# Kernel optimization log

Measured on AMD Instinct MI355X. Metric: run time of the kernel, lower is better.

## Reference

```python
import jax, jax.numpy as jnp
import numpy as np

DIM = 768
HEADS = 12
HEAD_DIM = DIM // HEADS
SCALE = HEAD_DIM ** -0.5
NEG = -65504.0


def setup_inputs() -> dict:
    key = jax.random.key(0)
    ks = jax.random.split(key, 7)
    B, N, C = 8, 1024, DIM
    x = jax.random.normal(ks[0], (B, N, C), dtype=jnp.float32)
    rel_pos_bias = jax.random.normal(ks[1], (HEADS, N, N), dtype=jnp.float32)
    attn_mask = jax.random.randint(ks[2], (B, N, N), 0, 2) == 1
    # parameters (torch nn.Linear: y = x @ W.T + b)
    W_qkv = jax.random.normal(ks[3], (3 * C, C), dtype=jnp.float32) * (C ** -0.5)
    b_qkv = jnp.zeros((3 * C,), dtype=jnp.float32)
    W_proj = jax.random.normal(ks[4], (C, C), dtype=jnp.float32) * (C ** -0.5)
    b_proj = jnp.zeros((C,), dtype=jnp.float32)
    return {"x": x, "rel_pos_bias": rel_pos_bias, "attn_mask": attn_mask,
            "W_qkv": W_qkv, "b_qkv": b_qkv, "W_proj": W_proj, "b_proj": b_proj}


def reference(x, rel_pos_bias, attn_mask, W_qkv, b_qkv, W_proj, b_proj):
    B, N, C = x.shape
    qkv = x @ W_qkv.T + b_qkv                                  # [B,N,3C]
    qkv = qkv.reshape(B, N, 3, HEADS, HEAD_DIM).transpose(2, 0, 3, 1, 4)
    q, k, v = qkv[0], qkv[1], qkv[2]                           # [B,H,N,D]
    attn = jnp.einsum('bhnd,bhmd->bhnm', q * SCALE, k)         # [B,H,N,N]
    attn = jnp.where(attn_mask[:, None, :, :], NEG, attn)
    attn = attn + rel_pos_bias[None]                           # bias broadcast over B
    attn_wo_softmax = attn
    p = jax.nn.softmax(attn, axis=-1)                          # attn_drop p=0 (eval)
    out = jnp.einsum('bhnm,bhmd->bhnd', p, v)
    out = out.transpose(0, 2, 1, 3).reshape(B, N, C)
    out = out @ W_proj.T + b_proj                              # proj_drop p=0
    return out, attn_wo_softmax
```

## Files before the change

kernel.cpp:

```cpp
#include <hip/hip_runtime.h>
#include <hip/hip_bf16.h>

typedef __attribute__((ext_vector_type(8))) short bf16x8;
typedef __attribute__((ext_vector_type(4))) short bf16x4;
typedef __attribute__((ext_vector_type(4))) float f32x4;

#define MFMA32(a,b,c) __builtin_amdgcn_mfma_f32_16x16x32_bf16(a,b,c,0,0,0)

#if __has_builtin(__builtin_amdgcn_mfma_f32_16x16x16bf16_1k)
#define MFMA16(a,b,c) __builtin_amdgcn_mfma_f32_16x16x16bf16_1k(a,b,c,0,0,0)
#else
static __device__ __forceinline__ f32x4 mfma16_asm(bf16x4 a, bf16x4 b, f32x4 c){
  asm volatile("v_mfma_f32_16x16x16_bf16 %0, %1, %2, %0" : "+v"(c) : "v"(a), "v"(b));
  return c;
}
#define MFMA16(a,b,c) mfma16_asm(a,b,c)
#endif

#define NEGV -65504.0f

__device__ __forceinline__ unsigned short f2bf(float f){
  union { float f; unsigned u; } x; x.f = f;
  unsigned r = x.u + 0x7fffu + ((x.u >> 16) & 1u);
  return (unsigned short)(r >> 16);
}

__device__ __forceinline__ unsigned cvtpk(float a, float b){
  unsigned r;
  asm volatile("v_cvt_pk_bf16_f32 %0, %1, %2" : "=v"(r) : "v"(a), "v"(b));
  return r;
}

__global__ void cvt_all(const float* __restrict__ x, const float* __restrict__ wq,
                        const float* __restrict__ wp, unsigned short* __restrict__ out){
  int i = blockIdx.x * 256 + threadIdx.x;
  const float* src; int j;
  if (i < 1572864)      { src = x;  j = i; }
  else if (i < 2015232) { src = wq; j = i - 1572864; }
  else                  { src = wp; j = i - 2015232; }
  float4 f = ((const float4*)src)[j];
  ushort4 u;
  u.x = f2bf(f.x); u.y = f2bf(f.y); u.z = f2bf(f.z); u.w = f2bf(f.w);
  ((ushort4*)out)[i] = u;
}

__global__ __launch_bounds__(256) void mask_to_bits(const int* __restrict__ m,
                                                    unsigned long long* __restrict__ out){
  int gw = (blockIdx.x * 256 + threadIdx.x) >> 6;
  int lane = threadIdx.x & 63;
#pragma unroll
  for (int stp = 0; stp < 16; ++stp) {
    size_t base = ((size_t)gw * 16 + stp) * 64;
    int v = m[base + lane];
    unsigned long long bb = __ballot(v != 0);
    if (lane == 0) out[base >> 6] = bb;
  }
}

__global__ __launch_bounds__(256) void gemm_qkv(
    const unsigned short* __restrict__ X,
    const unsigned short* __restrict__ W,
    const float* __restrict__ bias,
    unsigned short* __restrict__ Qd,
    unsigned short* __restrict__ Kd,
    unsigned short* __restrict__ Vd)
{
  __shared__ unsigned short As[128*40];
  __shared__ unsigned short Bs[128*40];
  const int K = 768;
  int tid = threadIdx.x;
  int bm = blockIdx.x & 63;
  int bn = blockIdx.x >> 6;
  int wave = tid >> 6, lane = tid & 63;
  int lo = lane & 15, g = lane >> 4;
  int wr = (wave >> 1) * 64, wc = (wave & 1) * 64;
  int row0 = bm * 128, col0 = bn * 128;

  int sr = tid >> 1;
  int sc = (tid & 1) * 16;
  const unsigned short* gA = X + (size_t)(row0 + sr) * K + sc;
  const unsigned short* gB = W + (size_t)(col0 + sr) * K + sc;
  unsigned short* sA = &As[sr * 40 + sc];
  unsigned short* sB = &Bs[sr * 40 + sc];

  f32x4 acc[4][4] = {};
  for (int k0 = 0; k0 < K; k0 += 32) {
    bf16x8 a0 = *(const bf16x8*)(gA + k0);
    bf16x8 a1 = *(const bf16x8*)(gA + k0 + 8);
    bf16x8 b0 = *(const bf16x8*)(gB + k0);
    bf16x8 b1 = *(const bf16x8*)(gB + k0 + 8);
    __syncthreads();
    *(bf16x8*)(sA)     = a0;
    *(bf16x8*)(sA + 8) = a1;
    *(bf16x8*)(sB)     = b0;
    *(bf16x8*)(sB + 8) = b1;
    __syncthreads();
    bf16x8 af[4], bf[4];
#pragma unroll
    for (int i = 0; i < 4; ++i) af[i] = *(const bf16x8*)&As[(wr + i*16 + lo)*40 + g*8];
#pragma unroll
    for (int i = 0; i < 4; ++i) bf[i] = *(const bf16x8*)&Bs[(wc + i*16 + lo)*40 + g*8];
#pragma unroll
    for (int mi = 0; mi < 4; ++mi)
#pragma unroll
      for (int ni = 0; ni < 4; ++ni)
        acc[mi][ni] = MFMA32(af[mi], bf[ni], acc[mi][ni]);
  }
  int orow0 = row0 + wr, ocol0 = col0 + wc;
#pragma unroll
  for (int ni = 0; ni < 4; ++ni) {
    int col = ocol0 + ni*16 + lo;
    float bc = bias[col];
    int which = col / 768;
    int rem = col - which * 768;
    int h = rem >> 6, d = rem & 63;
    unsigned short* dst = (which == 0) ? Qd : (which == 1) ? Kd : Vd;
    float scale = (which == 0) ? 0.125f : 1.0f;
#pragma unroll
    for (int mi = 0; mi < 4; ++mi) {
#pragma unroll
      for (int r = 0; r < 4; ++r) {
        int row = orow0 + mi*16 + g*4 + r;
        int bb = row >> 10, n = row & 1023;
        dst[(((size_t)bb*12 + h)*1024 + n)*64 + d] = f2bf((acc[mi][ni][r] + bc) * scale);
      }
    }
  }
}

__global__ __launch_bounds__(256) void vtrans(const unsigned short* __restrict__ V,
                                              unsigned short* __restrict__ Vt){
  __shared__ unsigned short t[64][72];
  int bh = blockIdx.y;
  int n0 = blockIdx.x * 64;
  int tid = threadIdx.x;
  int nl = tid >> 2;
  int dq = (tid & 3) * 16;
  const unsigned short* src = V + ((size_t)bh*1024 + n0 + nl)*64 + dq;
  bf16x8 a0 = *(const bf16x8*)(src);
  bf16x8 a1 = *(const bf16x8*)(src + 8);
  *(bf16x8*)&t[nl][dq]     = a0;
  *(bf16x8*)&t[nl][dq + 8] = a1;
  __syncthreads();
  int d  = tid >> 2;
  int nq = (tid & 3) * 16;
  union { unsigned short s[16]; bf16x8 v[2]; } pk;
#pragma unroll
  for (int j = 0; j < 16; ++j) pk.s[j] = t[nq + j][d];
  unsigned short* dst = Vt + ((size_t)bh*64 + d)*1024 + n0 + nq;
  *(bf16x8*)(dst)     = pk.v[0];
  *(bf16x8*)(dst + 8) = pk.v[1];
}

__global__ __launch_bounds__(512, 4) void attn_kernel(
    const unsigned short* __restrict__ Qd,
    const unsigned short* __restrict__ Kd,
    const unsigned short* __restrict__ Vt,
    const float* __restrict__ bias,
    const unsigned* __restrict__ maskbits,
    float* __restrict__ out1,
    unsigned short* __restrict__ ctx)
{
  __shared__ char lds[32768];
  const int N = 1024, D = 64;
  int y = blockIdx.y;
  int h = y >> 3, bb = y & 7;
  int bh = bb * 12 + h;
  int tid = threadIdx.x;
  int wave = tid >> 6, lane = tid & 63;
  int lo = lane & 15, g = lane >> 4;
  int qrow = blockIdx.x * 128 + wave * 16 + lo;

  const size_t qoff = ((size_t)bh * N + qrow) * D;
  bf16x8 qf0 = *(const bf16x8*)(Qd + qoff + g*8);
  bf16x8 qf1 = *(const bf16x8*)(Qd + qoff + 32 + g*8);

  const float* bias_row = bias + ((size_t)h * N + qrow) * N;
  const unsigned* mrow  = maskbits + ((size_t)bb * N + qrow) * 32;
  float* out_row        = out1 + ((size_t)bh * N + qrow) * N;

  int o  = tid * 16;
  int sw = o ^ (((o >> 7) & 7) << 4);
  const char* kbase = (const char*)(Kd + (size_t)bh * N * D);
  const char* vbase = (const char*)(Vt + (size_t)bh * D * N);
  const char* ksrc  = kbase + sw;
  const char* vsrc  = vbase + (o >> 7) * 2048 + (sw & 127);
  int wbase = (tid >> 6) << 10;

#define STAGE(buf, kv) do { \
    __builtin_amdgcn_global_load_lds( \
      (const __attribute__((address_space(1))) unsigned*)(ksrc + (size_t)(kv)*128), \
      (__attribute__((address_space(3))) unsigned*)(lds + (buf)*8192 + wbase), 16, 0, 0); \
    __builtin_amdgcn_global_load_lds( \
      (const __attribute__((address_space(1))) unsigned*)(vsrc + (size_t)(kv)*2), \
      (__attribute__((address_space(3))) unsigned*)(lds + 16384 + (buf)*8192 + wbase), 16, 0, 0); \
  } while (0)

#define SWZ(lb) ((lb) ^ ((((lb) >> 7) & 7) << 4))

  float m_run = -INFINITY, l_part = 0.0f;
  f32x4 oacc[4] = {};

  STAGE(0, 0);
  __syncthreads();
  int cur = 0;

  for (int it = 0; it < 16; ++it) {
    int kv = it * 64;
    if (it < 15) STAGE(cur ^ 1, kv + 64);
    __builtin_amdgcn_sched_barrier(0);

    unsigned mw0 = mrow[it*2];
    unsigned mw1 = mrow[it*2 + 1];

    f32x4 s[4];
    __builtin_amdgcn_s_setprio(1);
#pragma unroll
    for (int sub = 0; sub < 4; ++sub) {
      int lbr = (sub*16 + lo) * 128 + g*16;
      bf16x8 k0 = *(const bf16x8*)(lds + cur*8192 + SWZ(lbr));
      bf16x8 k1 = *(const bf16x8*)(lds + cur*8192 + SWZ(lbr + 64));
      f32x4 t = {};
      t = MFMA32(k0, qf0, t);
      t = MFMA32(k1, qf1, t);
      s[sub] = t;
    }
    __builtin_amdgcn_s_setprio(0);

    float sp[16];
#pragma unroll
    for (int sub = 0; sub < 4; ++sub) {
      f32x4 bi = *(const f32x4*)(bias_row + kv + sub*16 + g*4);
      unsigned mw = (sub < 2) ? mw0 : mw1;
      int sh = (sub & 1) * 16 + g * 4;
#pragma unroll
      for (int r = 0; r < 4; ++r)
        sp[sub*4+r] = (((mw >> (sh + r)) & 1u) ? NEGV : s[sub][r]) + bi[r];
      f32x4 ov;
      ov[0] = sp[sub*4]; ov[1] = sp[sub*4+1]; ov[2] = sp[sub*4+2]; ov[3] = sp[sub*4+3];
      __builtin_nontemporal_store(ov, (f32x4*)(out_row + kv + sub*16 + g*4));
    }

    float lmax = sp[0];
#pragma unroll
    for (int i = 1; i < 16; ++i) lmax = fmaxf(lmax, sp[i]);
    if (!__all(lmax <= m_run + 8.0f)) {
      float tmax = fmaxf(lmax, __shfl_xor(lmax, 16));
      tmax = fmaxf(tmax, __shfl_xor(tmax, 32));
      float mnew = fmaxf(m_run, tmax);
      float alpha = __expf(m_run - mnew);
      l_part *= alpha;
#pragma unroll
      for (int c = 0; c < 4; ++c) {
        oacc[c][0] *= alpha; oacc[c][1] *= alpha;
        oacc[c][2] *= alpha; oacc[c][3] *= alpha;
      }
      m_run = mnew;
    }
    float lsum = 0.0f;
#pragma unroll
    for (int i = 0; i < 16; ++i) { sp[i] = __expf(sp[i] - m_run); lsum += sp[i]; }
    l_part += lsum;

    union { unsigned u[2]; bf16x4 h; } pk[4];
#pragma unroll
    for (int ks = 0; ks < 4; ++ks) {
      pk[ks].u[0] = cvtpk(sp[ks*4],   sp[ks*4+1]);
      pk[ks].u[1] = cvtpk(sp[ks*4+2], sp[ks*4+3]);
    }

    __builtin_amdgcn_s_setprio(1);
#pragma unroll
    for (int ks = 0; ks < 4; ++ks)
#pragma unroll
      for (int c = 0; c < 4; ++c) {
        int lbv = (c*16 + lo) * 128 + ks*32 + g*8;
        bf16x4 vf = *(const bf16x4*)(lds + 16384 + cur*8192 + SWZ(lbv));
        oacc[c] = MFMA16(vf, pk[ks].h, oacc[c]);
      }
    __builtin_amdgcn_s_setprio(0);

    cur ^= 1;
    __builtin_amdgcn_sched_barrier(0);
    asm volatile("s_waitcnt vmcnt(4)" ::: "memory");
    __builtin_amdgcn_s_barrier();
  }

  l_part += __shfl_xor(l_part, 16);
  l_part += __shfl_xor(l_part, 32);
  float inv = 1.0f / l_part;

  size_t crow = ((size_t)bb * N + qrow) * 768 + h * 64;
#pragma unroll
  for (int c = 0; c < 4; ++c) {
    ushort4 u;
    u.x = f2bf(oacc[c][0] * inv);
    u.y = f2bf(oacc[c][1] * inv);
    u.z = f2bf(oacc[c][2] * inv);
    u.w = f2bf(oacc[c][3] * inv);
    *(ushort4*)(ctx + crow + c*16 + g*4) = u;
  }
#undef STAGE
#undef SWZ
}

__global__ __launch_bounds__(256) void gemm_proj(
    const unsigned short* __restrict__ X,
    const unsigned short* __restrict__ W,
    const float* __restrict__ bias,
    float* __restrict__ out)
{
  __shared__ unsigned short As[128*40];
  __shared__ unsigned short Bs[128*40];
  const int K = 768;
  int tid = threadIdx.x;
  int bm = blockIdx.x & 63;
  int bn = blockIdx.x >> 6;
  int wave = tid >> 6, lane = tid & 63;
  int lo = lane & 15, g = lane >> 4;
  int wr = (wave >> 1) * 64, wc = (wave & 1) * 64;
  int row0 = bm * 128, col0 = bn * 128;

  int sr = tid >> 1;
  int sc = (tid & 1) * 16;
  const unsigned short* gA = X + (size_t)(row0 + sr) * K + sc;
  const unsigned short* gB = W + (size_t)(col0 + sr) * K + sc;
  unsigned short* sA = &As[sr * 40 + sc];
  unsigned short* sB = &Bs[sr * 40 + sc];

  f32x4 acc[4][4] = {};
  for (int k0 = 0; k0 < K; k0 += 32) {
    bf16x8 a0 = *(const bf16x8*)(gA + k0);
    bf16x8 a1 = *(const bf16x8*)(gA + k0 + 8);
    bf16x8 b0 = *(const bf16x8*)(gB + k0);
    bf16x8 b1 = *(const bf16x8*)(gB + k0 + 8);
    __syncthreads();
    *(bf16x8*)(sA)     = a0;
    *(bf16x8*)(sA + 8) = a1;
    *(bf16x8*)(sB)     = b0;
    *(bf16x8*)(sB + 8) = b1;
    __syncthreads();
    bf16x8 af[4], bf[4];
#pragma unroll
    for (int i = 0; i < 4; ++i) af[i] = *(const bf16x8*)&As[(wr + i*16 + lo)*40 + g*8];
#pragma unroll
    for (int i = 0; i < 4; ++i) bf[i] = *(const bf16x8*)&Bs[(wc + i*16 + lo)*40 + g*8];
#pragma unroll
    for (int mi = 0; mi < 4; ++mi)
#pragma unroll
      for (int ni = 0; ni < 4; ++ni)
        acc[mi][ni] = MFMA32(af[mi], bf[ni], acc[mi][ni]);
  }
  int orow0 = row0 + wr, ocol0 = col0 + wc;
#pragma unroll
  for (int ni = 0; ni < 4; ++ni) {
    int col = ocol0 + ni*16 + lo;
    float bc = bias[col];
#pragma unroll
    for (int mi = 0; mi < 4; ++mi) {
#pragma unroll
      for (int r = 0; r < 4; ++r) {
        int row = orow0 + mi*16 + g*4 + r;
        out[(size_t)row * 768 + col] = acc[mi][ni][r] + bc;
      }
    }
  }
}

extern "C" void kernel_launch(void* const* d_in, const int* in_sizes, int n_in,
                              void* d_out, int out_size, void* d_ws, size_t ws_size,
                              hipStream_t stream) {
  const float* x            = (const float*)d_in[0];
  const float* rel_pos_bias = (const float*)d_in[1];
  const int* mask           = (const int*)d_in[2];
  const float* Wqkv         = (const float*)d_in[3];
  const float* bqkv         = (const float*)d_in[4];
  const float* Wproj        = (const float*)d_in[5];
  const float* bproj        = (const float*)d_in[6];

  float* out0 = (float*)d_out;
  float* out1 = out0 + (size_t)8 * 1024 * 768;

  char* ws = (char*)d_ws;
  unsigned short* xb  = (unsigned short*)(ws);
  unsigned short* wqb = (unsigned short*)(ws + 12582912);
  unsigned short* wpb = (unsigned short*)(ws + 16121856);
  unsigned short* Qb  = (unsigned short*)(ws + 17301504);
  unsigned short* Kb  = (unsigned short*)(ws + 29884416);
  unsigned short* Vb  = (unsigned short*)(ws + 42467328);
  unsigned short* ctx = (unsigned short*)(ws + 55050240);
  unsigned short* Vtb = xb;
  unsigned long long* mbits = (unsigned long long*)(ws + 12582912);

  cvt_all<<<8448, 256, 0, stream>>>(x, Wqkv, Wproj, xb);

  gemm_qkv<<<1152, 256, 0, stream>>>(xb, wqb, bqkv, Qb, Kb, Vb);

  mask_to_bits<<<2048, 256, 0, stream>>>(mask, mbits);

  vtrans<<<dim3(16, 96), 256, 0, stream>>>(Vb, Vtb);

  attn_kernel<<<dim3(8, 96), 512, 0, stream>>>(Qb, Kb, Vtb, rel_pos_bias,
                                               (const unsigned*)mbits, out1, ctx);

  gemm_proj<<<384, 256, 0, stream>>>(ctx, wpb, bproj, out0);
}
```

Measured before the change: 233.7 us.

## Pre-convert relative position bias to bf16 and prefetch bias and mask one tile ahead

Adds a kernel that converts rel_pos_bias to bf16 in workspace, so the attention kernel reads half the bias bytes on each of its eight per-batch passes. The attention kernel also loads the next tile's bias and mask words while the current tile is processed, with the wait count adjusted to match. This targets bias-read bandwidth and global-load latency. In exchange it adds a conversion pass over the bias, rounds the bias (and so the emitted pre-softmax scores) to bf16, and falls back to the fp32 path when the workspace is too small.

After: 246.5 us. +5.5%, slower.

```diff
diff --git a/kernel.cpp b/kernel.cpp
--- a/kernel.cpp
+++ b/kernel.cpp
@@ -25,20 +25,34 @@
   return (unsigned short)(r >> 16);
 }
 
+__device__ __forceinline__ float bf2f(unsigned short s){
+  union { unsigned u; float f; } c; c.u = ((unsigned)s) << 16; return c.f;
+}
+
 __device__ __forceinline__ unsigned cvtpk(float a, float b){
   unsigned r;
   asm volatile("v_cvt_pk_bf16_f32 %0, %1, %2" : "=v"(r) : "v"(a), "v"(b));
   return r;
 }
 
-__global__ void cvt_all(const float* __restrict__ x, const float* __restrict__ wq,
-                        const float* __restrict__ wp, unsigned short* __restrict__ out){
+__global__ __launch_bounds__(256) void cvt_all(
+    const float* __restrict__ x, const float* __restrict__ wq,
+    const float* __restrict__ wp, unsigned short* __restrict__ out){
   int i = blockIdx.x * 256 + threadIdx.x;
   const float* src; int j;
   if (i < 1572864)      { src = x;  j = i; }
   else if (i < 2015232) { src = wq; j = i - 1572864; }
   else                  { src = wp; j = i - 2015232; }
   float4 f = ((const float4*)src)[j];
+  ushort4 u;
+  u.x = f2bf(f.x); u.y = f2bf(f.y); u.z = f2bf(f.z); u.w = f2bf(f.w);
+  ((ushort4*)out)[i] = u;
+}
+
+__global__ __launch_bounds__(256) void cvt_bias(const float* __restrict__ in,
+                                                unsigned short* __restrict__ out){
+  int i = blockIdx.x * 256 + threadIdx.x;
+  float4 f = ((const float4*)in)[i];
   ushort4 u;
   u.x = f2bf(f.x); u.y = f2bf(f.y); u.z = f2bf(f.z); u.w = f2bf(f.w);
   ((ushort4*)out)[i] = u;
@@ -152,11 +166,12 @@
   *(bf16x8*)(dst + 8) = pk.v[1];
 }
 
+template<int BB>
 __global__ __launch_bounds__(512, 4) void attn_kernel(
     const unsigned short* __restrict__ Qd,
     const unsigned short* __restrict__ Kd,
     const unsigned short* __restrict__ Vt,
-    const float* __restrict__ bias,
+    const void* __restrict__ biasp,
     const unsigned* __restrict__ maskbits,
     float* __restrict__ out1,
     unsigned short* __restrict__ ctx)
@@ -175,7 +190,8 @@
   bf16x8 qf0 = *(const bf16x8*)(Qd + qoff + g*8);
   bf16x8 qf1 = *(const bf16x8*)(Qd + qoff + 32 + g*8);
 
-  const float* bias_row = bias + ((size_t)h * N + qrow) * N;
+  const float* brf = (const float*)biasp + ((size_t)h * N + qrow) * N;
+  const unsigned short* brh = (const unsigned short*)biasp + ((size_t)h * N + qrow) * N;
   const unsigned* mrow  = maskbits + ((size_t)bb * N + qrow) * 32;
   float* out_row        = out1 + ((size_t)bh * N + qrow) * N;
 
@@ -185,7 +201,7 @@
   const char* vbase = (const char*)(Vt + (size_t)bh * D * N);
   const char* ksrc  = kbase + sw;
   const char* vsrc  = vbase + (o >> 7) * 2048 + (sw & 127);
-  int wbase = (tid >> 6) << 10;
+  int wbase = wave << 10;
 
 #define STAGE(buf, kv) do { \
     __builtin_amdgcn_global_load_lds( \
@@ -198,20 +214,32 @@
 
 #define SWZ(lb) ((lb) ^ ((((lb) >> 7) & 7) << 4))
 
+#define LOADBIAS(kvx) do { \
+    if constexpr (BB) { \
+      _Pragma("unroll") for (int sub = 0; sub < 4; ++sub) \
+        bih[sub] = *(const bf16x4*)(brh + (kvx) + sub*16 + g*4); \
+    } else { \
+      _Pragma("unroll") for (int sub = 0; sub < 4; ++sub) \
+        bif[sub] = *(const f32x4*)(brf + (kvx) + sub*16 + g*4); \
+    } \
+  } while (0)
+
   float m_run = -INFINITY, l_part = 0.0f;
   f32x4 oacc[4] = {};
 
+  f32x4 bif[4]; bf16x4 bih[4];
+  uint2 mw = *(const uint2*)(mrow);
+  LOADBIAS(0);
   STAGE(0, 0);
   __syncthreads();
   int cur = 0;
 
   for (int it = 0; it < 16; ++it) {
     int kv = it * 64;
-    if (it < 15) STAGE(cur ^ 1, kv + 64);
+    int kvn = ((it + 1) & 15) << 6;
+
+    STAGE(cur ^ 1, kvn);
     __builtin_amdgcn_sched_barrier(0);
-
-    unsigned mw0 = mrow[it*2];
-    unsigned mw1 = mrow[it*2 + 1];
 
     f32x4 s[4];
     __builtin_amdgcn_s_setprio(1);
@@ -230,12 +258,22 @@
     float sp[16];
 #pragma unroll
     for (int sub = 0; sub < 4; ++sub) {
-      f32x4 bi = *(const f32x4*)(bias_row + kv + sub*16 + g*4);
-      unsigned mw = (sub < 2) ? mw0 : mw1;
+      unsigned mws = (sub < 2) ? mw.x : mw.y;
       int sh = (sub & 1) * 16 + g * 4;
 #pragma unroll
-      for (int r = 0; r < 4; ++r)
-        sp[sub*4+r] = (((mw >> (sh + r)) & 1u) ? NEGV : s[sub][r]) + bi[r];
+      for (int r = 0; r < 4; ++r) {
+        float bv = BB ? bf2f((unsigned short)bih[sub][r]) : bif[sub][r];
+        sp[sub*4+r] = (((mws >> (sh + r)) & 1u) ? NEGV : s[sub][r]) + bv;
+      }
+    }
+    __builtin_amdgcn_sched_barrier(0);
+
+    mw = *(const uint2*)(mrow + (kvn >> 5));
+    LOADBIAS(kvn);
+    __builtin_amdgcn_sched_barrier(0);
+
+#pragma unroll
+    for (int sub = 0; sub < 4; ++sub) {
       f32x4 ov;
       ov[0] = sp[sub*4]; ov[1] = sp[sub*4+1]; ov[2] = sp[sub*4+2]; ov[3] = sp[sub*4+3];
       __builtin_nontemporal_store(ov, (f32x4*)(out_row + kv + sub*16 + g*4));
@@ -262,7 +300,7 @@
     for (int i = 0; i < 16; ++i) { sp[i] = __expf(sp[i] - m_run); lsum += sp[i]; }
     l_part += lsum;
 
-    union { unsigned u[2]; bf16x4 h; } pk[4];
+    union { unsigned u[2]; bf16x4 hh; } pk[4];
 #pragma unroll
     for (int ks = 0; ks < 4; ++ks) {
       pk[ks].u[0] = cvtpk(sp[ks*4],   sp[ks*4+1]);
@@ -276,13 +314,13 @@
       for (int c = 0; c < 4; ++c) {
         int lbv = (c*16 + lo) * 128 + ks*32 + g*8;
         bf16x4 vf = *(const bf16x4*)(lds + 16384 + cur*8192 + SWZ(lbv));
-        oacc[c] = MFMA16(vf, pk[ks].h, oacc[c]);
+        oacc[c] = MFMA16(vf, pk[ks].hh, oacc[c]);
       }
     __builtin_amdgcn_s_setprio(0);
 
     cur ^= 1;
     __builtin_amdgcn_sched_barrier(0);
-    asm volatile("s_waitcnt vmcnt(4)" ::: "memory");
+    asm volatile("s_waitcnt vmcnt(9)" ::: "memory");
     __builtin_amdgcn_s_barrier();
   }
 
@@ -302,6 +340,7 @@
   }
 #undef STAGE
 #undef SWZ
+#undef LOADBIAS
 }
 
 __global__ __launch_bounds__(256) void gemm_proj(
@@ -390,9 +429,13 @@
   unsigned short* Vb  = (unsigned short*)(ws + 42467328);
   unsigned short* ctx = (unsigned short*)(ws + 55050240);
   unsigned short* Vtb = xb;
-  unsigned long long* mbits = (unsigned long long*)(ws + 12582912);
+  unsigned long long* mbits = (unsigned long long*)(ws + 67633152);
+  unsigned short* biasb = (unsigned short*)(ws + 68681728);
+
+  int big = ws_size >= (size_t)68681728 + 25165824;
 
   cvt_all<<<8448, 256, 0, stream>>>(x, Wqkv, Wproj, xb);
+  if (big) cvt_bias<<<12288, 256, 0, stream>>>(rel_pos_bias, biasb);
 
   gemm_qkv<<<1152, 256, 0, stream>>>(xb, wqb, bqkv, Qb, Kb, Vb);
 
@@ -400,8 +443,12 @@
 
   vtrans<<<dim3(16, 96), 256, 0, stream>>>(Vb, Vtb);
 
-  attn_kernel<<<dim3(8, 96), 512, 0, stream>>>(Qb, Kb, Vtb, rel_pos_bias,
-                                               (const unsigned*)mbits, out1, ctx);
+  if (big)
+    attn_kernel<1><<<dim3(8, 96), 512, 0, stream>>>(Qb, Kb, Vtb, (const void*)biasb,
+                                                    (const unsigned*)mbits, out1, ctx);
+  else
+    attn_kernel<0><<<dim3(8, 96), 512, 0, stream>>>(Qb, Kb, Vtb, (const void*)rel_pos_bias,
+                                                    (const unsigned*)mbits, out1, ctx);
 
   gemm_proj<<<384, 256, 0, stream>>>(ctx, wpb, bproj, out0);
 }
```
